# Kernel optimization log

Hardware: AMD Instinct MI355X
Metric: run time of the kernel (lower is better)

The kernel has to match this reference:

```python
import jax, jax.numpy as jnp
import numpy as np

B, C, O, H, W = 8, 256, 256, 64, 64
K = 3  # kernel size


def setup_inputs() -> dict:
    key = jax.random.key(0)
    k1, k2, k3 = jax.random.split(key, 3)
    x = jax.random.normal(k1, (B, C, H, W), dtype=jnp.float32)
    # offset-predicting conv: 18 = 2*K*K output channels (dy,dx per kernel tap).
    # Zero-init in the module; use small random weights so offsets are nontrivial.
    w_off = jax.random.normal(k2, (2 * K * K, C, K, K), dtype=jnp.float32) * 0.01
    b_off = jnp.zeros((2 * K * K,), dtype=jnp.float32)
    # deform conv weight, xavier-uniform (mmcv DeformConv has no bias)
    bound = float(np.sqrt(6.0 / (C * K * K + O * K * K)))
    w_def = jax.random.uniform(k3, (O, C, K, K), dtype=jnp.float32, minval=-bound, maxval=bound)
    return {"x": x, "w_off": w_off, "b_off": b_off, "w_def": w_def}


def _bilinear_gather(x, py, px):
    # x: [B,C,H,W]; py,px: [B,K2,Ho,Wo] float sample coords (zero padding outside)
    # returns [B,C,K2*Ho*Wo]
    Bb, Cc, Hh, Ww = x.shape
    y0f = jnp.floor(py); x0f = jnp.floor(px)
    wy = (py - y0f).reshape(Bb, 1, -1)
    wx = (px - x0f).reshape(Bb, 1, -1)
    y0 = y0f.astype(jnp.int32); x0 = x0f.astype(jnp.int32)
    flat = x.reshape(Bb, Cc, Hh * Ww)

    def gather(yi, xi):
        valid = ((yi >= 0) & (yi < Hh) & (xi >= 0) & (xi < Ww))
        yc = jnp.clip(yi, 0, Hh - 1); xc = jnp.clip(xi, 0, Ww - 1)
        idx = (yc * Ww + xc).reshape(Bb, 1, -1)
        g = jnp.take_along_axis(flat, jnp.broadcast_to(idx, (Bb, Cc, idx.shape[-1])), axis=2)
        return g * valid.reshape(Bb, 1, -1).astype(x.dtype)

    v00 = gather(y0, x0)
    v01 = gather(y0, x0 + 1)
    v10 = gather(y0 + 1, x0)
    v11 = gather(y0 + 1, x0 + 1)
    return (v00 * (1 - wy) * (1 - wx) + v01 * (1 - wy) * wx
            + v10 * wy * (1 - wx) + v11 * wy * wx)


def reference(x, w_off, b_off, w_def):
    # act -> offset conv -> deformable conv (norm = Identity)
    x = jax.nn.relu(x)
    offset = jax.lax.conv_general_dilated(
        x, w_off, (1, 1), ((1, 1), (1, 1)),
        dimension_numbers=('NCHW', 'OIHW', 'NCHW')) + b_off[None, :, None, None]
    Bb, Cc, Hh, Ww = x.shape
    Ho, Wo = offset.shape[2], offset.shape[3]
    K2 = K * K
    # mmcv offset layout: [B, 2*K2, H, W] with (dy, dx) pairs per kernel tap (row-major taps)
    off = offset.reshape(Bb, K2, 2, Ho, Wo)
    ky, kx = jnp.meshgrid(jnp.arange(K), jnp.arange(K), indexing='ij')
    ky = ky.reshape(-1).astype(x.dtype); kx = kx.reshape(-1).astype(x.dtype)
    # base sample positions: out_pos*stride - pad + tap  (stride=1, pad=1)
    base_y = jnp.arange(Ho, dtype=x.dtype)[None, :, None] - 1.0 + ky[:, None, None]  # [K2,Ho,1]
    base_x = jnp.arange(Wo, dtype=x.dtype)[None, None, :] - 1.0 + kx[:, None, None]  # [K2,1,Wo]
    py = base_y + off[:, :, 0]  # [B,K2,Ho,Wo]
    px = base_x + off[:, :, 1]
    samp = _bilinear_gather(x, py, px).reshape(Bb, Cc, K2, Ho, Wo)
    out = jnp.einsum('bckhw,ock->bohw', samp, w_def.reshape(w_def.shape[0], Cc, K2))
    return out
```

## Files before the change

kernel.cpp:

```cpp
#include <hip/hip_runtime.h>
#include <stdint.h>

#define B_ 8
#define C_ 256
#define O_ 256
#define HW_ 4096

typedef _Float16 f16x8 __attribute__((ext_vector_type(8)));
typedef __attribute__((ext_vector_type(4))) float f32x4;

__global__ __launch_bounds__(256) void k_nhwc(const float* __restrict__ x,
                                              _Float16* __restrict__ xT) {
    int bh = blockIdx.x;
    int b = bh & 7, h = bh >> 3;
    int t = threadIdx.x, px = t & 63, wg = t >> 6;
#pragma unroll
    for (int i = 0; i < 4; ++i) {
        int c0 = i * 64 + wg * 16;
        f16x8 va, vb;
#pragma unroll
        for (int j = 0; j < 8; ++j) {
            float f0 = x[((size_t)(b * C_ + c0 + j)) * HW_ + h * 64 + px];
            float f1 = x[((size_t)(b * C_ + c0 + 8 + j)) * HW_ + h * 64 + px];
            va[j] = (_Float16)fmaxf(f0, 0.f);
            vb[j] = (_Float16)fmaxf(f1, 0.f);
        }
        _Float16* dst = xT + ((size_t)((b * 64 + h) * 64 + px)) * C_ + c0;
        *reinterpret_cast<f16x8*>(dst) = va;
        *reinterpret_cast<f16x8*>(dst + 8) = vb;
    }
}

__global__ void k_prep_wdef(const float* __restrict__ w_def, _Float16* __restrict__ wfrag) {
    int idx = blockIdx.x * 256 + threadIdx.x;
    if (idx >= 9 * 8 * 16 * 64) return;
    int lane = idx & 63;
    int mfg = (idx >> 6) & 15;
    int ccc = (idx >> 10) & 7;
    int k2 = idx >> 13;
    int o = mfg * 16 + (lane & 15);
    int cb = ccc * 32 + (lane >> 4) * 8;
    f16x8 pk;
#pragma unroll
    for (int j = 0; j < 8; ++j)
        pk[j] = (_Float16)w_def[(size_t)(o * C_ + cb + j) * 9 + k2];
    *reinterpret_cast<f16x8*>(wfrag + (size_t)idx * 8) = pk;
}

__global__ void k_prep_woffrag(const float* __restrict__ w_off, _Float16* __restrict__ wfr) {
    int idx = blockIdx.x * 256 + threadIdx.x;
    if (idx >= 9 * 8 * 2 * 64) return;
    int lane = idx & 63;
    int mfg = (idx >> 6) & 1;
    int ccc = (idx >> 7) & 7;
    int k2 = idx >> 10;
    int o = mfg * 16 + (lane & 15);
    int cb = ccc * 32 + (lane >> 4) * 8;
    f16x8 pk;
#pragma unroll
    for (int j = 0; j < 8; ++j)
        pk[j] = (o < 18) ? (_Float16)w_off[(size_t)(o * C_ + cb + j) * 9 + k2] : (_Float16)0.f;
    *reinterpret_cast<f16x8*>(wfr + (size_t)idx * 8) = pk;
}

__global__ __launch_bounds__(256) void k_offconv4(const _Float16* __restrict__ xT,
                                                  const _Float16* __restrict__ wofr,
                                                  const float* __restrict__ b_off,
                                                  float* __restrict__ offs) {
    int bh = blockIdx.x;
    int b = bh & 7, h = bh >> 3;
    int tid = threadIdx.x, lane = tid & 63, wm = tid >> 6;
    int px = wm * 16 + (lane & 15);
    int chl = (lane >> 4) * 8;
    f32x4 acc0 = (f32x4){0.f, 0.f, 0.f, 0.f};
    f32x4 acc1 = (f32x4){0.f, 0.f, 0.f, 0.f};
    const _Float16* xb = xT + (size_t)b * HW_ * C_;
    for (int k2 = 0; k2 < 9; ++k2) {
        int y = h + k2 / 3 - 1;
        int xs = px + k2 % 3 - 1;
        bool v = ((unsigned)y < 64u) && ((unsigned)xs < 64u);
        int yc = y < 0 ? 0 : (y > 63 ? 63 : y);
        int xc = xs < 0 ? 0 : (xs > 63 ? 63 : xs);
        const _Float16* xp = xb + (size_t)(yc * 64 + xc) * C_ + chl;
#pragma unroll
        for (int q = 0; q < 8; ++q) {
            f16x8 bf = *reinterpret_cast<const f16x8*>(xp + q * 32);
            if (!v) bf = (f16x8)(_Float16)0.f;
            const f16x8* wp = reinterpret_cast<const f16x8*>(wofr) +
                              (size_t)((k2 * 8 + q) * 2) * 64 + lane;
            acc0 = __builtin_amdgcn_mfma_f32_16x16x32_f16(wp[0], bf, acc0, 0, 0, 0);
            acc1 = __builtin_amdgcn_mfma_f32_16x16x32_f16(wp[64], bf, acc1, 0, 0, 0);
        }
    }
#pragma unroll
    for (int r = 0; r < 4; ++r) {
        int oc = (lane >> 4) * 4 + r;
        offs[(((size_t)b * 18 + oc) * 64 + h) * 64 + px] = acc0[r] + b_off[oc];
    }
#pragma unroll
    for (int r = 0; r < 4; ++r) {
        int oc = 16 + (lane >> 4) * 4 + r;
        if (oc < 18)
            offs[(((size_t)b * 18 + oc) * 64 + h) * 64 + px] = acc1[r] + b_off[oc];
    }
}

__global__ __launch_bounds__(256, 3) void k_deform6(const _Float16* __restrict__ xT,
                                                    const _Float16* __restrict__ wfrag,
                                                    const float* __restrict__ offs,
                                                    float* __restrict__ out) {
    int blk = blockIdx.x;
    int b = blk & 7, h = blk >> 3;
    int tid = threadIdx.x, lane = tid & 63, wm = tid >> 6;
    int gp = tid & 63, gq = tid >> 6;

    __shared__ float s_py[9][64], s_px[9][64];
    __shared__ __align__(16) _Float16 s_x[7 * 64 * 40];
    __shared__ __align__(16) _Float16 s_samp[2][64 * 40];

    const _Float16* xb = xT + (size_t)b * HW_ * C_;

    for (int idx = tid; idx < 576; idx += 256) {
        int k2 = idx >> 6, p = idx & 63;
        float dy = offs[(((size_t)b * 18 + k2 * 2 + 0) * 64 + h) * 64 + p];
        float dx = offs[(((size_t)b * 18 + k2 * 2 + 1) * 64 + h) * 64 + p];
        s_py[k2][p] = (float)(h - 1 + k2 / 3) + dy;
        s_px[k2][p] = (float)(p - 1 + k2 % 3) + dx;
    }
    __syncthreads();

    f32x4 acc[4][4];
#pragma unroll
    for (int i = 0; i < 4; ++i)
#pragma unroll
        for (int j = 0; j < 4; ++j) acc[i][j] = (f32x4){0.f, 0.f, 0.f, 0.f};

#define LOADA(DST, T)                                                              \
    {                                                                              \
        const f16x8* wf = reinterpret_cast<const f16x8*>(wfrag) +                  \
                          ((size_t)(T) * 16 + wm * 4) * 64 + lane;                 \
        _Pragma("unroll") for (int mf = 0; mf < 4; ++mf) DST[mf] = wf[mf * 64];    \
    }

#define PACKSTEP(K2, BUF)                                                          \
    {                                                                              \
        float py = s_py[K2][gp], pxx = s_px[K2][gp];                               \
        float y0f = floorf(py), x0f = floorf(pxx);                                 \
        float wy = py - y0f, wx = pxx - x0f;                                       \
        int y0 = (int)y0f, x0 = (int)x0f;                                          \
        float w00 = (1.f - wy) * (1.f - wx), w01 = (1.f - wy) * wx;                \
        float w10 = wy * (1.f - wx), w11 = wy * wx;                                \
        bool vy0 = (unsigned)y0 < 64u, vy1 = (unsigned)(y0 + 1) < 64u;             \
        bool vx0 = (unsigned)x0 < 64u, vx1 = (unsigned)(x0 + 1) < 64u;             \
        if (!(vy0 && vx0)) w00 = 0.f;                                              \
        if (!(vy0 && vx1)) w01 = 0.f;                                              \
        if (!(vy1 && vx0)) w10 = 0.f;                                              \
        if (!(vy1 && vx1)) w11 = 0.f;                                              \
        _Float16 hw00 = (_Float16)w00, hw01 = (_Float16)w01;                       \
        _Float16 hw10 = (_Float16)w10, hw11 = (_Float16)w11;                       \
        int x0c = x0 < 0 ? 0 : (x0 > 63 ? 63 : x0);                                \
        int x1c = (x0 + 1) < 0 ? 0 : ((x0 + 1) > 63 ? 63 : (x0 + 1));              \
        int ry0 = y0 - h + 3;                                                      \
        f16x8 c00, c01, c10, c11;                                                  \
        if (ry0 >= 0 && ry0 <= 5) {                                                \
            const _Float16* base0 = s_x + ry0 * 2560 + gq * 8;                     \
            c00 = *reinterpret_cast<const f16x8*>(base0 + x0c * 40);               \
            c01 = *reinterpret_cast<const f16x8*>(base0 + x1c * 40);               \
            c10 = *reinterpret_cast<const f16x8*>(base0 + 2560 + x0c * 40);        \
            c11 = *reinterpret_cast<const f16x8*>(base0 + 2560 + x1c * 40);        \
        } else {                                                                   \
            int y0c = y0 < 0 ? 0 : (y0 > 63 ? 63 : y0);                            \
            int y1c = (y0 + 1) < 0 ? 0 : ((y0 + 1) > 63 ? 63 : (y0 + 1));          \
            const _Float16* gb = xb + cq * 32 + gq * 8;                            \
            c00 = *reinterpret_cast<const f16x8*>(gb + (size_t)(y0c * 64 + x0c) * C_); \
            c01 = *reinterpret_cast<const f16x8*>(gb + (size_t)(y0c * 64 + x1c) * C_); \
            c10 = *reinterpret_cast<const f16x8*>(gb + (size_t)(y1c * 64 + x0c) * C_); \
            c11 = *reinterpret_cast<const f16x8*>(gb + (size_t)(y1c * 64 + x1c) * C_); \
        }                                                                          \
        f16x8 pk = c00 * hw00 + c01 * hw01 + c10 * hw10 + c11 * hw11;              \
        *reinterpret_cast<f16x8*>(&s_samp[BUF][gp * 40 + gq * 8]) = pk;            \
    }

    f16x8 Ac[4], An[4];
    LOADA(Ac, 0);
#pragma unroll
    for (int mf = 0; mf < 4; ++mf) An[mf] = Ac[mf];

    for (int cq = 0; cq < 8; ++cq) {
        {
            int spx = tid >> 2, o = tid & 3;
#pragma unroll
            for (int r = 0; r < 7; ++r) {
                int yr = h - 3 + r;
                yr = yr < 0 ? 0 : (yr > 63 ? 63 : yr);
                f16x8 v = *reinterpret_cast<const f16x8*>(
                    xb + (size_t)(yr * 64 + spx) * C_ + cq * 32 + o * 8);
                *reinterpret_cast<f16x8*>(&s_x[(r * 64 + spx) * 40 + o * 8]) = v;
            }
        }
        asm volatile("s_waitcnt lgkmcnt(0)" ::: "memory");
        __builtin_amdgcn_s_barrier();

        PACKSTEP(0, 0);
        asm volatile("s_waitcnt lgkmcnt(0)" ::: "memory");
        __builtin_amdgcn_s_barrier();

#pragma unroll
        for (int k2 = 0; k2 < 9; ++k2) {
            if (k2 < 8) {
                LOADA(An, (k2 + 1) * 8 + cq);
            } else if (cq < 7) {
                LOADA(An, cq + 1);
            }

            f16x8 bfr[4];
#pragma unroll
            for (int nf = 0; nf < 4; ++nf) {
                int n = nf * 16 + (lane & 15);
                bfr[nf] = *reinterpret_cast<const f16x8*>(
                    &s_samp[k2 & 1][n * 40 + (lane >> 4) * 8]);
            }

#pragma unroll
            for (int mf = 0; mf < 4; ++mf)
#pragma unroll
                for (int nf = 0; nf < 4; ++nf)
                    acc[mf][nf] = __builtin_amdgcn_mfma_f32_16x16x32_f16(
                        Ac[mf], bfr[nf], acc[mf][nf], 0, 0, 0);

            if (k2 < 8) {
                PACKSTEP(k2 + 1, (k2 + 1) & 1);
            }
#pragma unroll
            for (int mf = 0; mf < 4; ++mf) Ac[mf] = An[mf];

            asm volatile("s_waitcnt lgkmcnt(0)" ::: "memory");
            __builtin_amdgcn_s_barrier();
        }
    }

    float* op = out + (size_t)b * O_ * HW_ + h * 64;
#pragma unroll
    for (int mf = 0; mf < 4; ++mf)
#pragma unroll
        for (int nf = 0; nf < 4; ++nf)
#pragma unroll
            for (int r = 0; r < 4; ++r) {
                int o = wm * 64 + mf * 16 + (lane >> 4) * 4 + r;
                int w = nf * 16 + (lane & 15);
                op[(size_t)o * HW_ + w] = acc[mf][nf][r];
            }
}

extern "C" void kernel_launch(void* const* d_in, const int* in_sizes, int n_in,
                              void* d_out, int out_size, void* d_ws, size_t ws_size,
                              hipStream_t stream) {
    const float* x = (const float*)d_in[0];
    const float* w_off = (const float*)d_in[1];
    const float* b_off = (const float*)d_in[2];
    const float* w_def = (const float*)d_in[3];
    float* out = (float*)d_out;
    char* ws = (char*)d_ws;

    float* offs = (float*)ws;
    _Float16* xT = (_Float16*)(ws + 2359296);
    _Float16* wfrag = (_Float16*)(ws + 2359296 + 16777216);
    _Float16* wofr = (_Float16*)(ws + 2359296 + 16777216 + 1179648);

    k_nhwc<<<512, 256, 0, stream>>>(x, xT);
    k_prep_wdef<<<288, 256, 0, stream>>>(w_def, wfrag);
    k_prep_woffrag<<<36, 256, 0, stream>>>(w_off, wofr);
    k_offconv4<<<512, 256, 0, stream>>>(xT, wofr, b_off, offs);
    k_deform6<<<512, 256, 0, stream>>>(xT, wfrag, offs, out);
}
```

Measured before the change: 106.6 us.

## Restructure deform kernel: per-wave pixel slices, register-built samples, precomputed bilinear tables

Each wave now computes all 256 output channels for 16 pixels and builds its bilinear-sampled B fragment directly in registers. This removes the shared sample buffer and the per-tap barriers. Bilinear weights and clamped indices are precomputed once per block into LDS tables, and the next channel chunk of x rows is prefetched into registers while the current one computes. In exchange, each wave streams the full weight fragment set from global memory per tap, and occupancy is lowered to 2 blocks per CU.

```diff
diff --git a/kernel.cpp b/kernel.cpp
--- a/kernel.cpp
+++ b/kernel.cpp
@@ -105,18 +105,18 @@
     }
 }
 
-__global__ __launch_bounds__(256, 3) void k_deform6(const _Float16* __restrict__ xT,
+__global__ __launch_bounds__(256, 2) void k_deform7(const _Float16* __restrict__ xT,
                                                     const _Float16* __restrict__ wfrag,
                                                     const float* __restrict__ offs,
                                                     float* __restrict__ out) {
     int blk = blockIdx.x;
     int b = blk & 7, h = blk >> 3;
     int tid = threadIdx.x, lane = tid & 63, wm = tid >> 6;
-    int gp = tid & 63, gq = tid >> 6;
-
-    __shared__ float s_py[9][64], s_px[9][64];
+
+    __shared__ unsigned s_w00[576], s_w01[576], s_w10[576], s_w11[576];
+    __shared__ unsigned s_xx[576];
+    __shared__ unsigned s_yy[576];
     __shared__ __align__(16) _Float16 s_x[7 * 64 * 40];
-    __shared__ __align__(16) _Float16 s_samp[2][64 * 40];
 
     const _Float16* xb = xT + (size_t)b * HW_ * C_;
 
@@ -124,132 +124,119 @@
         int k2 = idx >> 6, p = idx & 63;
         float dy = offs[(((size_t)b * 18 + k2 * 2 + 0) * 64 + h) * 64 + p];
         float dx = offs[(((size_t)b * 18 + k2 * 2 + 1) * 64 + h) * 64 + p];
-        s_py[k2][p] = (float)(h - 1 + k2 / 3) + dy;
-        s_px[k2][p] = (float)(p - 1 + k2 % 3) + dx;
-    }
-    __syncthreads();
-
-    f32x4 acc[4][4];
-#pragma unroll
-    for (int i = 0; i < 4; ++i)
-#pragma unroll
-        for (int j = 0; j < 4; ++j) acc[i][j] = (f32x4){0.f, 0.f, 0.f, 0.f};
-
-#define LOADA(DST, T)                                                              \
+        float py = (float)(h - 1 + k2 / 3) + dy;
+        float pxx = (float)(p - 1 + k2 % 3) + dx;
+        float y0f = floorf(py), x0f = floorf(pxx);
+        float wy = py - y0f, wx = pxx - x0f;
+        int y0 = (int)y0f, x0 = (int)x0f;
+        float w00 = (1.f - wy) * (1.f - wx), w01 = (1.f - wy) * wx;
+        float w10 = wy * (1.f - wx), w11 = wy * wx;
+        bool vy0 = (unsigned)y0 < 64u, vy1 = (unsigned)(y0 + 1) < 64u;
+        bool vx0 = (unsigned)x0 < 64u, vx1 = (unsigned)(x0 + 1) < 64u;
+        if (!(vy0 && vx0)) w00 = 0.f;
+        if (!(vy0 && vx1)) w01 = 0.f;
+        if (!(vy1 && vx0)) w10 = 0.f;
+        if (!(vy1 && vx1)) w11 = 0.f;
+        union { _Float16 h[2]; unsigned u; } cv;
+#define DUP(W) (cv.h[0] = (_Float16)(W), cv.h[1] = cv.h[0], cv.u)
+        s_w00[idx] = DUP(w00);
+        s_w01[idx] = DUP(w01);
+        s_w10[idx] = DUP(w10);
+        s_w11[idx] = DUP(w11);
+#undef DUP
+        int x0c = x0 < 0 ? 0 : (x0 > 63 ? 63 : x0);
+        int x1c = (x0 + 1) < 0 ? 0 : ((x0 + 1) > 63 ? 63 : (x0 + 1));
+        int y0c = y0 < 0 ? 0 : (y0 > 63 ? 63 : y0);
+        int y1c = (y0 + 1) < 0 ? 0 : ((y0 + 1) > 63 ? 63 : (y0 + 1));
+        int ry0 = y0 - (h - 3);
+        unsigned flag = (ry0 >= 0 && ry0 <= 5) ? (unsigned)ry0 : 255u;
+        s_xx[idx] = (unsigned)x0c | ((unsigned)x1c << 16);
+        s_yy[idx] = (unsigned)y0c | ((unsigned)y1c << 8) | (flag << 16);
+    }
+
+    f32x4 acc[16];
+#pragma unroll
+    for (int i = 0; i < 16; ++i) acc[i] = (f32x4){0.f, 0.f, 0.f, 0.f};
+
+    int spx = tid >> 2, so = tid & 3;
+    f16x8 st[7];
+#define STAGE_LOAD(CQ)                                                             \
     {                                                                              \
-        const f16x8* wf = reinterpret_cast<const f16x8*>(wfrag) +                  \
-                          ((size_t)(T) * 16 + wm * 4) * 64 + lane;                 \
-        _Pragma("unroll") for (int mf = 0; mf < 4; ++mf) DST[mf] = wf[mf * 64];    \
-    }
-
-#define PACKSTEP(K2, BUF)                                                          \
+        _Pragma("unroll") for (int r = 0; r < 7; ++r)                              \
+        {                                                                          \
+            int yr = h - 3 + r;                                                    \
+            yr = yr < 0 ? 0 : (yr > 63 ? 63 : yr);                                 \
+            st[r] = *reinterpret_cast<const f16x8*>(                               \
+                xb + (size_t)(yr * 64 + spx) * C_ + (CQ) * 32 + so * 8);           \
+        }                                                                          \
+    }
+#define STAGE_WRITE()                                                              \
     {                                                                              \
-        float py = s_py[K2][gp], pxx = s_px[K2][gp];                               \
-        float y0f = floorf(py), x0f = floorf(pxx);                                 \
-        float wy = py - y0f, wx = pxx - x0f;                                       \
-        int y0 = (int)y0f, x0 = (int)x0f;                                          \
-        float w00 = (1.f - wy) * (1.f - wx), w01 = (1.f - wy) * wx;                \
-        float w10 = wy * (1.f - wx), w11 = wy * wx;                                \
-        bool vy0 = (unsigned)y0 < 64u, vy1 = (unsigned)(y0 + 1) < 64u;             \
-        bool vx0 = (unsigned)x0 < 64u, vx1 = (unsigned)(x0 + 1) < 64u;             \
-        if (!(vy0 && vx0)) w00 = 0.f;                                              \
-        if (!(vy0 && vx1)) w01 = 0.f;                                              \
-        if (!(vy1 && vx0)) w10 = 0.f;                                              \
-        if (!(vy1 && vx1)) w11 = 0.f;                                              \
-        _Float16 hw00 = (_Float16)w00, hw01 = (_Float16)w01;                       \
-        _Float16 hw10 = (_Float16)w10, hw11 = (_Float16)w11;                       \
-        int x0c = x0 < 0 ? 0 : (x0 > 63 ? 63 : x0);                                \
-        int x1c = (x0 + 1) < 0 ? 0 : ((x0 + 1) > 63 ? 63 : (x0 + 1));              \
-        int ry0 = y0 - h + 3;                                                      \
-        f16x8 c00, c01, c10, c11;                                                  \
-        if (ry0 >= 0 && ry0 <= 5) {                                                \
-            const _Float16* base0 = s_x + ry0 * 2560 + gq * 8;                     \
-            c00 = *reinterpret_cast<const f16x8*>(base0 + x0c * 40);               \
-            c01 = *reinterpret_cast<const f16x8*>(base0 + x1c * 40);               \
-            c10 = *reinterpret_cast<const f16x8*>(base0 + 2560 + x0c * 40);        \
-            c11 = *reinterpret_cast<const f16x8*>(base0 + 2560 + x1c * 40);        \
-        } else {                                                                   \
-            int y0c = y0 < 0 ? 0 : (y0 > 63 ? 63 : y0);                            \
-            int y1c = (y0 + 1) < 0 ? 0 : ((y0 + 1) > 63 ? 63 : (y0 + 1));          \
-            const _Float16* gb = xb + cq * 32 + gq * 8;                            \
-            c00 = *reinterpret_cast<const f16x8*>(gb + (size_t)(y0c * 64 + x0c) * C_); \
-            c01 = *reinterpret_cast<const f16x8*>(gb + (size_t)(y0c * 64 + x1c) * C_); \
-            c10 = *reinterpret_cast<const f16x8*>(gb + (size_t)(y1c * 64 + x0c) * C_); \
-            c11 = *reinterpret_cast<const f16x8*>(gb + (size_t)(y1c * 64 + x1c) * C_); \
-        }                                                                          \
-        f16x8 pk = c00 * hw00 + c01 * hw01 + c10 * hw10 + c11 * hw11;              \
-        *reinterpret_cast<f16x8*>(&s_samp[BUF][gp * 40 + gq * 8]) = pk;            \
-    }
-
-    f16x8 Ac[4], An[4];
-    LOADA(Ac, 0);
-#pragma unroll
-    for (int mf = 0; mf < 4; ++mf) An[mf] = Ac[mf];
+        _Pragma("unroll") for (int r = 0; r < 7; ++r)                              \
+            *reinterpret_cast<f16x8*>(&s_x[(r * 64 + spx) * 40 + so * 8]) = st[r]; \
+    }
+
+    STAGE_LOAD(0);
+    STAGE_WRITE();
+    asm volatile("s_waitcnt lgkmcnt(0)" ::: "memory");
+    __builtin_amdgcn_s_barrier();
+
+    int pl = lane & 15;
+    int oc8 = (lane >> 4) * 8;
 
     for (int cq = 0; cq < 8; ++cq) {
-        {
-            int spx = tid >> 2, o = tid & 3;
-#pragma unroll
-            for (int r = 0; r < 7; ++r) {
-                int yr = h - 3 + r;
-                yr = yr < 0 ? 0 : (yr > 63 ? 63 : yr);
-                f16x8 v = *reinterpret_cast<const f16x8*>(
-                    xb + (size_t)(yr * 64 + spx) * C_ + cq * 32 + o * 8);
-                *reinterpret_cast<f16x8*>(&s_x[(r * 64 + spx) * 40 + o * 8]) = v;
+        if (cq < 7) STAGE_LOAD(cq + 1);
+
+#pragma unroll
+        for (int k2 = 0; k2 < 9; ++k2) {
+            int g = k2 * 64 + wm * 16 + pl;
+            union { unsigned u; _Float16 h[2]; } uw0, uw1, uw2, uw3;
+            uw0.u = s_w00[g]; uw1.u = s_w01[g]; uw2.u = s_w10[g]; uw3.u = s_w11[g];
+            unsigned xx = s_xx[g], yy = s_yy[g];
+            int x0c = xx & 0xFFFF, x1c = xx >> 16;
+            int flag = yy >> 16;
+            f16x8 c00, c01, c10, c11;
+            if (flag <= 5) {
+                const _Float16* base0 = s_x + flag * 2560 + oc8;
+                c00 = *reinterpret_cast<const f16x8*>(base0 + x0c * 40);
+                c01 = *reinterpret_cast<const f16x8*>(base0 + x1c * 40);
+                c10 = *reinterpret_cast<const f16x8*>(base0 + 2560 + x0c * 40);
+                c11 = *reinterpret_cast<const f16x8*>(base0 + 2560 + x1c * 40);
+            } else {
+                int y0c = yy & 0xFF, y1c = (yy >> 8) & 0xFF;
+                const _Float16* gb = xb + cq * 32 + oc8;
+                c00 = *reinterpret_cast<const f16x8*>(gb + (size_t)(y0c * 64 + x0c) * C_);
+                c01 = *reinterpret_cast<const f16x8*>(gb + (size_t)(y0c * 64 + x1c) * C_);
+                c10 = *reinterpret_cast<const f16x8*>(gb + (size_t)(y1c * 64 + x0c) * C_);
+                c11 = *reinterpret_cast<const f16x8*>(gb + (size_t)(y1c * 64 + x1c) * C_);
             }
-        }
-        asm volatile("s_waitcnt lgkmcnt(0)" ::: "memory");
-        __builtin_amdgcn_s_barrier();
-
-        PACKSTEP(0, 0);
-        asm volatile("s_waitcnt lgkmcnt(0)" ::: "memory");
-        __builtin_amdgcn_s_barrier();
-
-#pragma unroll
-        for (int k2 = 0; k2 < 9; ++k2) {
-            if (k2 < 8) {
-                LOADA(An, (k2 + 1) * 8 + cq);
-            } else if (cq < 7) {
-                LOADA(An, cq + 1);
+            f16x8 pk = c00 * uw0.h[0] + c01 * uw1.h[0] + c10 * uw2.h[0] + c11 * uw3.h[0];
+
+            const f16x8* wf = reinterpret_cast<const f16x8*>(wfrag) +
+                              ((size_t)(k2 * 8 + cq) * 16) * 64 + lane;
+#pragma unroll
+            for (int mf = 0; mf < 16; ++mf) {
+                f16x8 af = wf[(size_t)mf * 64];
+                acc[mf] = __builtin_amdgcn_mfma_f32_16x16x32_f16(af, pk, acc[mf], 0, 0, 0);
             }
-
-            f16x8 bfr[4];
-#pragma unroll
-            for (int nf = 0; nf < 4; ++nf) {
-                int n = nf * 16 + (lane & 15);
-                bfr[nf] = *reinterpret_cast<const f16x8*>(
-                    &s_samp[k2 & 1][n * 40 + (lane >> 4) * 8]);
-            }
-
-#pragma unroll
-            for (int mf = 0; mf < 4; ++mf)
-#pragma unroll
-                for (int nf = 0; nf < 4; ++nf)
-                    acc[mf][nf] = __builtin_amdgcn_mfma_f32_16x16x32_f16(
-                        Ac[mf], bfr[nf], acc[mf][nf], 0, 0, 0);
-
-            if (k2 < 8) {
-                PACKSTEP(k2 + 1, (k2 + 1) & 1);
-            }
-#pragma unroll
-            for (int mf = 0; mf < 4; ++mf) Ac[mf] = An[mf];
-
+        }
+
+        if (cq < 7) {
+            __builtin_amdgcn_s_barrier();
+            STAGE_WRITE();
             asm volatile("s_waitcnt lgkmcnt(0)" ::: "memory");
             __builtin_amdgcn_s_barrier();
         }
     }
 
-    float* op = out + (size_t)b * O_ * HW_ + h * 64;
-#pragma unroll
-    for (int mf = 0; mf < 4; ++mf)
-#pragma unroll
-        for (int nf = 0; nf < 4; ++nf)
-#pragma unroll
-            for (int r = 0; r < 4; ++r) {
-                int o = wm * 64 + mf * 16 + (lane >> 4) * 4 + r;
-                int w = nf * 16 + (lane & 15);
-                op[(size_t)o * HW_ + w] = acc[mf][nf][r];
-            }
+    float* op = out + (size_t)b * O_ * HW_ + h * 64 + wm * 16 + pl;
+#pragma unroll
+    for (int mf = 0; mf < 16; ++mf)
+#pragma unroll
+        for (int r = 0; r < 4; ++r) {
+            int o = mf * 16 + (lane >> 4) * 4 + r;
+            op[(size_t)o * HW_] = acc[mf][r];
+        }
 }
 
 extern "C" void kernel_launch(void* const* d_in, const int* in_sizes, int n_in,
@@ -271,5 +258,5 @@
     k_prep_wdef<<<288, 256, 0, stream>>>(w_def, wfrag);
     k_prep_woffrag<<<36, 256, 0, stream>>>(w_off, wofr);
     k_offconv4<<<512, 256, 0, stream>>>(xT, wofr, b_off, offs);
-    k_deform6<<<512, 256, 0, stream>>>(xT, wfrag, offs, out);
-}
+    k_deform7<<<512, 256, 0, stream>>>(xT, wfrag, offs, out);
+}
```

Result: slower. 190.1 us (+78.3%).

## Prefetch next channel slab into registers and precompute bilinear geometry once

Applied to the files above, without the earlier changes.

The deform kernel now issues global loads for the next 32-channel x slab into registers during the current slab's MFMA loop, then writes them to shared memory after the loop. This hides global latency that was previously exposed at the start of each slab. Bilinear weights, clamped indices and the in-window flag are computed once per tap and packed into a shared uint4 table, instead of being recomputed in every slab iteration. Launch bounds drop from 3 to 2 blocks per SM to make room for the extra staging registers, which may reduce occupancy.

```diff
diff --git a/kernel.cpp b/kernel.cpp
--- a/kernel.cpp
+++ b/kernel.cpp
@@ -105,7 +105,7 @@
     }
 }
 
-__global__ __launch_bounds__(256, 3) void k_deform6(const _Float16* __restrict__ xT,
+__global__ __launch_bounds__(256, 2) void k_deform8(const _Float16* __restrict__ xT,
                                                     const _Float16* __restrict__ wfrag,
                                                     const float* __restrict__ offs,
                                                     float* __restrict__ out) {
@@ -114,20 +114,69 @@
     int tid = threadIdx.x, lane = tid & 63, wm = tid >> 6;
     int gp = tid & 63, gq = tid >> 6;
 
-    __shared__ float s_py[9][64], s_px[9][64];
+    __shared__ uint4 s_geo[576];
     __shared__ __align__(16) _Float16 s_x[7 * 64 * 40];
     __shared__ __align__(16) _Float16 s_samp[2][64 * 40];
 
     const _Float16* xb = xT + (size_t)b * HW_ * C_;
+
+    int spx = tid >> 2, so = tid & 3;
+    f16x8 st[7];
+#define STAGE_LOAD(CQ)                                                             \
+    {                                                                              \
+        _Pragma("unroll") for (int r = 0; r < 7; ++r)                              \
+        {                                                                          \
+            int yr = h - 3 + r;                                                    \
+            yr = yr < 0 ? 0 : (yr > 63 ? 63 : yr);                                 \
+            st[r] = *reinterpret_cast<const f16x8*>(                               \
+                xb + (size_t)(yr * 64 + spx) * C_ + (CQ) * 32 + so * 8);           \
+        }                                                                          \
+    }
+#define STAGE_WRITE()                                                              \
+    {                                                                              \
+        _Pragma("unroll") for (int r = 0; r < 7; ++r)                              \
+            *reinterpret_cast<f16x8*>(&s_x[(r * 64 + spx) * 40 + so * 8]) = st[r]; \
+    }
+
+    STAGE_LOAD(0);
 
     for (int idx = tid; idx < 576; idx += 256) {
         int k2 = idx >> 6, p = idx & 63;
         float dy = offs[(((size_t)b * 18 + k2 * 2 + 0) * 64 + h) * 64 + p];
         float dx = offs[(((size_t)b * 18 + k2 * 2 + 1) * 64 + h) * 64 + p];
-        s_py[k2][p] = (float)(h - 1 + k2 / 3) + dy;
-        s_px[k2][p] = (float)(p - 1 + k2 % 3) + dx;
-    }
-    __syncthreads();
+        float py = (float)(h - 1 + k2 / 3) + dy;
+        float pxx = (float)(p - 1 + k2 % 3) + dx;
+        float y0f = floorf(py), x0f = floorf(pxx);
+        float wy = py - y0f, wx = pxx - x0f;
+        int y0 = (int)y0f, x0 = (int)x0f;
+        float w00 = (1.f - wy) * (1.f - wx), w01 = (1.f - wy) * wx;
+        float w10 = wy * (1.f - wx), w11 = wy * wx;
+        bool vy0 = (unsigned)y0 < 64u, vy1 = (unsigned)(y0 + 1) < 64u;
+        bool vx0 = (unsigned)x0 < 64u, vx1 = (unsigned)(x0 + 1) < 64u;
+        if (!(vy0 && vx0)) w00 = 0.f;
+        if (!(vy0 && vx1)) w01 = 0.f;
+        if (!(vy1 && vx0)) w10 = 0.f;
+        if (!(vy1 && vx1)) w11 = 0.f;
+        union { _Float16 h[2]; unsigned u; } p01, p23;
+        p01.h[0] = (_Float16)w00; p01.h[1] = (_Float16)w01;
+        p23.h[0] = (_Float16)w10; p23.h[1] = (_Float16)w11;
+        int x0c = x0 < 0 ? 0 : (x0 > 63 ? 63 : x0);
+        int x1c = (x0 + 1) < 0 ? 0 : ((x0 + 1) > 63 ? 63 : (x0 + 1));
+        int y0c = y0 < 0 ? 0 : (y0 > 63 ? 63 : y0);
+        int y1c = (y0 + 1) < 0 ? 0 : ((y0 + 1) > 63 ? 63 : (y0 + 1));
+        int ry0 = y0 - (h - 3);
+        unsigned flag = (ry0 >= 0 && ry0 <= 5) ? (unsigned)ry0 : 255u;
+        uint4 g;
+        g.x = p01.u;
+        g.y = p23.u;
+        g.z = (unsigned)x0c | ((unsigned)x1c << 16);
+        g.w = (unsigned)y0c | ((unsigned)y1c << 8) | (flag << 16);
+        s_geo[idx] = g;
+    }
+
+    STAGE_WRITE();
+    asm volatile("s_waitcnt lgkmcnt(0)" ::: "memory");
+    __builtin_amdgcn_s_barrier();
 
     f32x4 acc[4][4];
 #pragma unroll
@@ -142,42 +191,29 @@
         _Pragma("unroll") for (int mf = 0; mf < 4; ++mf) DST[mf] = wf[mf * 64];    \
     }
 
-#define PACKSTEP(K2, BUF)                                                          \
+#define PACKSTEP(K2, BUF, CQ)                                                      \
     {                                                                              \
-        float py = s_py[K2][gp], pxx = s_px[K2][gp];                               \
-        float y0f = floorf(py), x0f = floorf(pxx);                                 \
-        float wy = py - y0f, wx = pxx - x0f;                                       \
-        int y0 = (int)y0f, x0 = (int)x0f;                                          \
-        float w00 = (1.f - wy) * (1.f - wx), w01 = (1.f - wy) * wx;                \
-        float w10 = wy * (1.f - wx), w11 = wy * wx;                                \
-        bool vy0 = (unsigned)y0 < 64u, vy1 = (unsigned)(y0 + 1) < 64u;             \
-        bool vx0 = (unsigned)x0 < 64u, vx1 = (unsigned)(x0 + 1) < 64u;             \
-        if (!(vy0 && vx0)) w00 = 0.f;                                              \
-        if (!(vy0 && vx1)) w01 = 0.f;                                              \
-        if (!(vy1 && vx0)) w10 = 0.f;                                              \
-        if (!(vy1 && vx1)) w11 = 0.f;                                              \
-        _Float16 hw00 = (_Float16)w00, hw01 = (_Float16)w01;                       \
-        _Float16 hw10 = (_Float16)w10, hw11 = (_Float16)w11;                       \
-        int x0c = x0 < 0 ? 0 : (x0 > 63 ? 63 : x0);                                \
-        int x1c = (x0 + 1) < 0 ? 0 : ((x0 + 1) > 63 ? 63 : (x0 + 1));              \
-        int ry0 = y0 - h + 3;                                                      \
+        uint4 gg = s_geo[(K2) * 64 + gp];                                          \
+        union { unsigned u; _Float16 h[2]; } p01, p23;                             \
+        p01.u = gg.x; p23.u = gg.y;                                                \
+        int x0c = gg.z & 0xFFFF, x1c = gg.z >> 16;                                 \
+        int flag = gg.w >> 16;                                                     \
         f16x8 c00, c01, c10, c11;                                                  \
-        if (ry0 >= 0 && ry0 <= 5) {                                                \
-            const _Float16* base0 = s_x + ry0 * 2560 + gq * 8;                     \
+        if (flag <= 5) {                                                           \
+            const _Float16* base0 = s_x + flag * 2560 + gq * 8;                    \
             c00 = *reinterpret_cast<const f16x8*>(base0 + x0c * 40);               \
             c01 = *reinterpret_cast<const f16x8*>(base0 + x1c * 40);               \
             c10 = *reinterpret_cast<const f16x8*>(base0 + 2560 + x0c * 40);        \
             c11 = *reinterpret_cast<const f16x8*>(base0 + 2560 + x1c * 40);        \
         } else {                                                                   \
-            int y0c = y0 < 0 ? 0 : (y0 > 63 ? 63 : y0);                            \
-            int y1c = (y0 + 1) < 0 ? 0 : ((y0 + 1) > 63 ? 63 : (y0 + 1));          \
-            const _Float16* gb = xb + cq * 32 + gq * 8;                            \
+            int y0c = gg.w & 0xFF, y1c = (gg.w >> 8) & 0xFF;                       \
+            const _Float16* gb = xb + (CQ) * 32 + gq * 8;                          \
             c00 = *reinterpret_cast<const f16x8*>(gb + (size_t)(y0c * 64 + x0c) * C_); \
             c01 = *reinterpret_cast<const f16x8*>(gb + (size_t)(y0c * 64 + x1c) * C_); \
             c10 = *reinterpret_cast<const f16x8*>(gb + (size_t)(y1c * 64 + x0c) * C_); \
             c11 = *reinterpret_cast<const f16x8*>(gb + (size_t)(y1c * 64 + x1c) * C_); \
         }                                                                          \
-        f16x8 pk = c00 * hw00 + c01 * hw01 + c10 * hw10 + c11 * hw11;              \
+        f16x8 pk = c00 * p01.h[0] + c01 * p01.h[1] + c10 * p23.h[0] + c11 * p23.h[1]; \
         *reinterpret_cast<f16x8*>(&s_samp[BUF][gp * 40 + gq * 8]) = pk;            \
     }
 
@@ -187,23 +223,11 @@
     for (int mf = 0; mf < 4; ++mf) An[mf] = Ac[mf];
 
     for (int cq = 0; cq < 8; ++cq) {
-        {
-            int spx = tid >> 2, o = tid & 3;
-#pragma unroll
-            for (int r = 0; r < 7; ++r) {
-                int yr = h - 3 + r;
-                yr = yr < 0 ? 0 : (yr > 63 ? 63 : yr);
-                f16x8 v = *reinterpret_cast<const f16x8*>(
-                    xb + (size_t)(yr * 64 + spx) * C_ + cq * 32 + o * 8);
-                *reinterpret_cast<f16x8*>(&s_x[(r * 64 + spx) * 40 + o * 8]) = v;
-            }
-        }
+        PACKSTEP(0, 0, cq);
         asm volatile("s_waitcnt lgkmcnt(0)" ::: "memory");
         __builtin_amdgcn_s_barrier();
 
-        PACKSTEP(0, 0);
-        asm volatile("s_waitcnt lgkmcnt(0)" ::: "memory");
-        __builtin_amdgcn_s_barrier();
+        if (cq < 7) STAGE_LOAD(cq + 1);
 
 #pragma unroll
         for (int k2 = 0; k2 < 9; ++k2) {
@@ -228,12 +252,16 @@
                     acc[mf][nf] = __builtin_amdgcn_mfma_f32_16x16x32_f16(
                         Ac[mf], bfr[nf], acc[mf][nf], 0, 0, 0);
 
-            if (k2 < 8) {
-                PACKSTEP(k2 + 1, (k2 + 1) & 1);
-            }
+            if (k2 < 8) PACKSTEP(k2 + 1, (k2 + 1) & 1, cq);
 #pragma unroll
             for (int mf = 0; mf < 4; ++mf) Ac[mf] = An[mf];
 
+            asm volatile("s_waitcnt lgkmcnt(0)" ::: "memory");
+            __builtin_amdgcn_s_barrier();
+        }
+
+        if (cq < 7) {
+            STAGE_WRITE();
             asm volatile("s_waitcnt lgkmcnt(0)" ::: "memory");
             __builtin_amdgcn_s_barrier();
         }
@@ -271,5 +299,5 @@
     k_prep_wdef<<<288, 256, 0, stream>>>(w_def, wfrag);
     k_prep_woffrag<<<36, 256, 0, stream>>>(w_off, wofr);
     k_offconv4<<<512, 256, 0, stream>>>(xT, wofr, b_off, offs);
-    k_deform6<<<512, 256, 0, stream>>>(xT, wfrag, offs, out);
-}
+    k_deform8<<<512, 256, 0, stream>>>(xT, wfrag, offs, out);
+}
```

After: 106.2 us. Within noise of the previous version (-0.4%).
